# Kernel tuning notes

Measured on AMD Instinct MI355X. Metric: run time of the kernel, lower is better.

The kernel has to match this reference:

```python
import jax, jax.numpy as jnp
import numpy as np

B, S, E, H = 2, 2048, 1024, 16
D = E // H

def setup_inputs() -> dict:
    key = jax.random.key(0)
    ks = jax.random.split(key, 11)
    sc = 0.02
    inp = {
        'queries': jax.random.normal(ks[0], (B, S, E), jnp.float32),
        'keys':    jax.random.normal(ks[1], (B, S, E), jnp.float32),
        'values':  jax.random.normal(ks[2], (B, S, E), jnp.float32),
        'Wq': jax.random.normal(ks[3], (E, E), jnp.float32) * sc,
        'bq': jnp.zeros((E,), jnp.float32),
        'Wk': jax.random.normal(ks[4], (E, E), jnp.float32) * sc,
        'bk': jnp.zeros((E,), jnp.float32),
        'Wv': jax.random.normal(ks[5], (E, E), jnp.float32) * sc,
        'bv': jnp.zeros((E,), jnp.float32),
        'Wo': jax.random.normal(ks[6], (E, E), jnp.float32) * sc,
        'bo': jnp.zeros((E,), jnp.float32),
        'indicator': 0,
    }
    return inp

def reference(queries, keys, values, Wq, bq, Wk, bk, Wv, bv, Wo, bo, indicator):
    # torch Linear: y = x @ W.T + b
    q = queries @ Wq.T + bq
    k = keys    @ Wk.T + bk
    v = values  @ Wv.T + bv
    # [B,S,E] -> [B,H,S,D]
    q = q.reshape(B, S, H, D).transpose(0, 2, 1, 3)
    k = k.reshape(B, S, H, D).transpose(0, 2, 1, 3)
    v = v.reshape(B, S, H, D).transpose(0, 2, 1, 3)
    scores = jnp.einsum('bhqd,bhkd->bhqk', q, k) / jnp.sqrt(jnp.float32(D))
    w = jax.nn.sigmoid(scores)
    if indicator != 0:
        w = 1.0 - w
    attn = jax.nn.softmax(w, axis=-1)  # dropout_prob=0 -> identity
    out = jnp.einsum('bhqk,bhkd->bhqd', attn, v)
    out = out.transpose(0, 2, 1, 3).reshape(B, S, E)
    return out @ Wo.T + bo
```

## Files before the change

### kernel.cpp

```cpp
#include <hip/hip_runtime.h>
#include <stdint.h>

#define Bb 2
#define Ss 2048
#define Ee 1024
#define Hh 16
#define Dd 64

typedef __bf16 bf16;
typedef __attribute__((ext_vector_type(8))) __bf16 bf16x8;
typedef __attribute__((ext_vector_type(4))) __bf16 bf16x4;
typedef __attribute__((ext_vector_type(4))) float f32x4;

#define MB (1u << 20)
#define OFF_XQ 0u
#define OFF_XK (8u * MB)
#define OFF_XV (16u * MB)
#define OFF_WQ (24u * MB)
#define OFF_WK (26u * MB)
#define OFF_WV (28u * MB)
#define OFF_WO (30u * MB)
#define OFF_Q  (32u * MB)
#define OFF_K  (40u * MB)
#define OFF_VT (48u * MB)
#define OFF_AO (56u * MB)

__device__ __forceinline__ void gll16(const void* g, void* lds) {
  __builtin_amdgcn_global_load_lds(
      (const __attribute__((address_space(1))) void*)g,
      (__attribute__((address_space(3))) void*)lds, 16, 0, 0);
}

__device__ __forceinline__ unsigned pkbf(float lo, float hi) {
  unsigned r;
  asm("v_cvt_pk_bf16_f32 %0, %1, %2" : "=v"(r) : "v"(lo), "v"(hi));
  return r;
}
#define PL32SWAP(a, b) asm("v_permlane32_swap_b32 %0, %1" : "+v"(a), "+v"(b))
#define PL16SWAP(a, b) asm("v_permlane16_swap_b32 %0, %1" : "+v"(a), "+v"(b))

__global__ __launch_bounds__(256) void convert_kernel(
    const float* __restrict__ q, const float* __restrict__ k, const float* __restrict__ v,
    const float* __restrict__ wq, const float* __restrict__ wk, const float* __restrict__ wv,
    const float* __restrict__ wo, const int* __restrict__ ind, char* __restrict__ ws)
{
  const unsigned i = blockIdx.x * 256u + threadIdx.x;
  const float* src;
  bf16* dst;
  float scale = 1.0f;
  if (i < 3145728u) {
    const unsigned a = i >> 20, j = i & 1048575u;
    src = (a == 0 ? q : a == 1 ? k : v) + (size_t)j * 4;
    dst = (bf16*)(ws + (size_t)a * (8u * MB)) + (size_t)j * 4;
  } else {
    const unsigned i2 = i - 3145728u;
    const unsigned a = i2 >> 18, j = i2 & 262143u;
    src = (a == 0 ? wq : a == 1 ? wk : a == 2 ? wv : wo) + (size_t)j * 4;
    dst = (bf16*)(ws + OFF_WQ + (size_t)a * (2u * MB)) + (size_t)j * 4;
    if (a == 0) {
      const float c1v = (*ind != 0) ? 1.442695041f : -1.442695041f;
      scale = 0.125f * c1v;
    }
  }
  const float4 f = *(const float4*)src;
  bf16x4 o;
  o[0] = (bf16)(f.x * scale);
  o[1] = (bf16)(f.y * scale);
  o[2] = (bf16)(f.z * scale);
  o[3] = (bf16)(f.w * scale);
  *(bf16x4*)dst = o;
}

template <bool TR>
__device__ __forceinline__ void gemm128_body(
    const bf16* __restrict__ A, const bf16* __restrict__ W,
    char* smem, int m0, int n0, int t, f32x4 (&acc)[4][4])
{
  char* As = smem;
  char* Bs = smem + 16384;
  const int lane = t & 63;
  const int wid = t >> 6;
  const int wm = (wid >> 1) << 6;
  const int wn = (wid & 1) << 6;
  for (int kt = 0; kt < 1024; kt += 64) {
    __syncthreads();
#pragma unroll
    for (int i = 0; i < 4; ++i) {
      const int L = i * 4096 + t * 16;
      const int r = L >> 7;
      const int c = ((L >> 4) & 7) ^ (r & 7);
      gll16(A + (size_t)(m0 + r) * 1024 + kt + c * 8, As + i * 4096 + wid * 1024);
      gll16(W + (size_t)(n0 + r) * 1024 + kt + c * 8, Bs + i * 4096 + wid * 1024);
    }
    __syncthreads();
#pragma unroll
    for (int ks = 0; ks < 2; ++ks) {
      bf16x8 af[4], bff[4];
#pragma unroll
      for (int mi = 0; mi < 4; ++mi) {
        const int r = wm + mi * 16 + (lane & 15);
        const int c = (ks * 4 + (lane >> 4)) ^ (r & 7);
        af[mi] = *(const bf16x8*)(As + r * 128 + c * 16);
      }
#pragma unroll
      for (int ni = 0; ni < 4; ++ni) {
        const int r = wn + ni * 16 + (lane & 15);
        const int c = (ks * 4 + (lane >> 4)) ^ (r & 7);
        bff[ni] = *(const bf16x8*)(Bs + r * 128 + c * 16);
      }
      __builtin_amdgcn_s_setprio(1);
#pragma unroll
      for (int mi = 0; mi < 4; ++mi)
#pragma unroll
        for (int ni = 0; ni < 4; ++ni) {
          if (TR)
            acc[mi][ni] = __builtin_amdgcn_mfma_f32_16x16x32_bf16(bff[ni], af[mi], acc[mi][ni], 0, 0, 0);
          else
            acc[mi][ni] = __builtin_amdgcn_mfma_f32_16x16x32_bf16(af[mi], bff[ni], acc[mi][ni], 0, 0, 0);
        }
      __builtin_amdgcn_s_setprio(0);
    }
  }
}

__global__ __launch_bounds__(256) void proj_gemm(
    char* __restrict__ ws, const float* __restrict__ bq,
    const float* __restrict__ bk, const float* __restrict__ bv,
    const int* __restrict__ ind)
{
  __shared__ __align__(16) char smem[32768];
  const int zi = blockIdx.z;
  const bf16* A = (const bf16*)(ws + (zi == 0 ? OFF_XQ : zi == 1 ? OFF_XK : OFF_XV));
  const bf16* W = (const bf16*)(ws + (zi == 0 ? OFF_WQ : zi == 1 ? OFF_WK : OFF_WV));
  const float* bias = zi == 0 ? bq : zi == 1 ? bk : bv;
  bf16* outp = (bf16*)(ws + (zi == 0 ? OFF_Q : zi == 1 ? OFF_K : OFF_VT));
  const float c1v = (*ind != 0) ? 1.442695041f : -1.442695041f;
  const float bscale = (zi == 0) ? 0.125f * c1v : 1.0f;
  const int t = threadIdx.x;
  const int m0 = blockIdx.y * 128, n0 = blockIdx.x * 128;
  const int lane = t & 63, wid = t >> 6;
  const int wm = (wid >> 1) << 6, wn = (wid & 1) << 6;
  const int l15 = lane & 15, g = lane >> 4;
  f32x4 acc[4][4] = {};
  if (zi == 2) {
    gemm128_body<false>(A, W, smem, m0, n0, t, acc);
#pragma unroll
    for (int ni = 0; ni < 4; ++ni) {
      const int col = n0 + wn + ni * 16 + l15;
      const float bvv = bias[col];
      const int h = col >> 6, d = col & 63;
#pragma unroll
      for (int mi = 0; mi < 4; ++mi) {
        const int row0 = m0 + wm + mi * 16 + g * 4;
        const int b = row0 >> 11, s = row0 & 2047;
        bf16x4 o;
#pragma unroll
        for (int r2 = 0; r2 < 4; ++r2) o[r2] = (bf16)(acc[mi][ni][r2] + bvv);
        *(bf16x4*)&outp[((size_t)((b * Hh + h) * Dd + d) * Ss) + s] = o;
      }
    }
  } else {
    gemm128_body<true>(A, W, smem, m0, n0, t, acc);
#pragma unroll
    for (int mi = 0; mi < 4; ++mi) {
      const int row = m0 + wm + mi * 16 + l15;
      const int b = row >> 11, s = row & 2047;
#pragma unroll
      for (int ni = 0; ni < 4; ++ni) {
        const int col0 = n0 + wn + ni * 16 + g * 4;
        const int h = col0 >> 6, d0 = col0 & 63;
        const float4 b4 = *(const float4*)&bias[col0];
        bf16x4 o;
        o[0] = (bf16)(acc[mi][ni][0] + b4.x * bscale);
        o[1] = (bf16)(acc[mi][ni][1] + b4.y * bscale);
        o[2] = (bf16)(acc[mi][ni][2] + b4.z * bscale);
        o[3] = (bf16)(acc[mi][ni][3] + b4.w * bscale);
        *(bf16x4*)&outp[((size_t)((b * Hh + h) * Ss + s) * Dd) + d0] = o;
      }
    }
  }
}

__global__ __launch_bounds__(256, 4) void attn_kernel(char* __restrict__ ws)
{
  __shared__ __align__(16) char smem[32768];
  char* Ks  = smem;
  char* Vts = smem + 16384;
  char* Os  = smem;
  const int t = threadIdx.x, lane = t & 63, wid = t >> 6;
  const int g = lane >> 4, l15 = lane & 15;
  const int lin = blockIdx.x;
  const int bh = ((lin & 7) << 2) + ((lin >> 3) & 3);
  const int q0 = (lin >> 5) << 6;
  const bf16* Qg  = (const bf16*)(ws + OFF_Q)  + (size_t)bh * Ss * Dd;
  const bf16* Kg  = (const bf16*)(ws + OFF_K)  + (size_t)bh * Ss * Dd;
  const bf16* Vtg = (const bf16*)(ws + OFF_VT) + (size_t)bh * Ss * Dd;
  bf16* AO = (bf16*)(ws + OFF_AO);

  bf16x8 qf[2];
#pragma unroll
  for (int ks = 0; ks < 2; ++ks)
    qf[ks] = *(const bf16x8*)(Qg + (size_t)(q0 + wid * 16 + l15) * Dd + ks * 32 + g * 8);

  f32x4 acc_o[4] = {};
  f32x4 acc_sum = {};
  union { unsigned u[4]; bf16x8 v; } ones_;
#pragma unroll
  for (int j = 0; j < 4; ++j) ones_.u[j] = 0x3F803F80u;

  for (int kt = 0; kt < Ss; kt += 128) {
    __syncthreads();
#pragma unroll
    for (int i = 0; i < 4; ++i) {
      const int L = i * 4096 + t * 16;
      const int r = L >> 7;
      const int c = ((L >> 4) & 7) ^ (r & 7);
      gll16(Kg + (size_t)(kt + r) * Dd + c * 8, Ks + i * 4096 + wid * 1024);
    }
#pragma unroll
    for (int i = 0; i < 4; ++i) {
      const int L = i * 4096 + t * 16;
      const int r = L >> 8;
      const int c = ((L >> 4) & 15) ^ (r & 15);
      gll16(Vtg + (size_t)r * Ss + kt + c * 8, Vts + i * 4096 + wid * 1024);
    }
    __syncthreads();

    f32x4 st[8];
#pragma unroll
    for (int ni = 0; ni < 8; ++ni)
      st[ni] = (f32x4){-0.52876637f, -0.52876637f, -0.52876637f, -0.52876637f};
    __builtin_amdgcn_s_setprio(1);
#pragma unroll
    for (int ks = 0; ks < 2; ++ks) {
#pragma unroll
      for (int ni = 0; ni < 8; ++ni) {
        const int r = ni * 16 + l15;
        const int c = (ks * 4 + g) ^ (r & 7);
        const bf16x8 kf = *(const bf16x8*)(Ks + r * 128 + c * 16);
        st[ni] = __builtin_amdgcn_mfma_f32_16x16x32_bf16(kf, qf[ks], st[ni], 0, 0, 0);
      }
    }
    __builtin_amdgcn_s_setprio(0);

#pragma unroll
    for (int kb = 0; kb < 4; ++kb) {
      float p[2][4];
#pragma unroll
      for (int e = 0; e < 2; ++e)
#pragma unroll
        for (int r2 = 0; r2 < 4; ++r2) {
          const float ex = __builtin_amdgcn_exp2f(st[2 * kb + e][r2]);
          const float tt = __builtin_amdgcn_rcpf(0.69314718f + ex);
          p[e][r2] = __builtin_amdgcn_exp2f(tt);
        }
      unsigned E0 = pkbf(p[0][0], p[0][1]);
      unsigned E1 = pkbf(p[0][2], p[0][3]);
      unsigned O0 = pkbf(p[1][0], p[1][1]);
      unsigned O1 = pkbf(p[1][2], p[1][3]);
      PL32SWAP(E0, O0);
      PL16SWAP(E0, O0);
      PL32SWAP(E1, O1);
      PL16SWAP(E1, O1);
      union { unsigned u[4]; bf16x8 v; } pb;
      pb.u[0] = E0; pb.u[1] = E1; pb.u[2] = O0; pb.u[3] = O1;
      __builtin_amdgcn_s_setprio(1);
#pragma unroll
      for (int dblk = 0; dblk < 4; ++dblk) {
        const int r = dblk * 16 + l15;
        const int c = (kb * 4 + g) ^ (r & 15);
        const bf16x8 vf = *(const bf16x8*)(Vts + r * 256 + c * 16);
        acc_o[dblk] = __builtin_amdgcn_mfma_f32_16x16x32_bf16(vf, pb.v, acc_o[dblk], 0, 0, 0);
      }
      acc_sum = __builtin_amdgcn_mfma_f32_16x16x32_bf16(ones_.v, pb.v, acc_sum, 0, 0, 0);
      __builtin_amdgcn_s_setprio(0);
    }
  }

  const float rinv = __builtin_amdgcn_rcpf(acc_sum[0]);

  __syncthreads();
  {
    const int row = wid * 16 + l15;
#pragma unroll
    for (int dblk = 0; dblk < 4; ++dblk) {
      const unsigned w0 = pkbf(acc_o[dblk][0] * rinv, acc_o[dblk][1] * rinv);
      const unsigned w1 = pkbf(acc_o[dblk][2] * rinv, acc_o[dblk][3] * rinv);
      const int cc = dblk * 2 + (g >> 1);
      char* a = Os + row * 128 + (cc ^ (row & 7)) * 16 + (g & 1) * 8;
      *(uint2*)a = make_uint2(w0, w1);
    }
  }
  __syncthreads();
  const int b = bh >> 4, h = bh & 15;
#pragma unroll
  for (int i = 0; i < 2; ++i) {
    const int L = i * 4096 + t * 16;
    const int r = L >> 7;
    const int cc = (L >> 4) & 7;
    const uint4 w = *(const uint4*)(Os + r * 128 + (cc ^ (r & 7)) * 16);
    *(uint4*)&AO[((size_t)(b * Ss + q0 + r) << 10) + h * 64 + cc * 8] = w;
  }
}

__global__ __launch_bounds__(256) void out_gemm(char* __restrict__ ws,
                                                const float* __restrict__ bo,
                                                float* __restrict__ outp)
{
  __shared__ __align__(16) char smem[24576];
  char* As = smem;
  char* Bs = smem + 16384;
  const bf16* A = (const bf16*)(ws + OFF_AO);
  const bf16* W = (const bf16*)(ws + OFF_WO);
  const int t = threadIdx.x, lane = t & 63, wid = t >> 6;
  const int l15 = lane & 15, g = lane >> 4;
  const int m0 = blockIdx.y * 128, n0 = blockIdx.x * 64;
  const int wm = (wid >> 1) << 6;
  const int wn = (wid & 1) << 5;
  f32x4 acc[4][2] = {};
  for (int kt = 0; kt < 1024; kt += 64) {
    __syncthreads();
#pragma unroll
    for (int i = 0; i < 4; ++i) {
      const int L = i * 4096 + t * 16;
      const int r = L >> 7;
      const int c = ((L >> 4) & 7) ^ (r & 7);
      gll16(A + (size_t)(m0 + r) * 1024 + kt + c * 8, As + i * 4096 + wid * 1024);
    }
#pragma unroll
    for (int i = 0; i < 2; ++i) {
      const int L = i * 4096 + t * 16;
      const int r = L >> 7;
      const int c = ((L >> 4) & 7) ^ (r & 7);
      gll16(W + (size_t)(n0 + r) * 1024 + kt + c * 8, Bs + i * 4096 + wid * 1024);
    }
    __syncthreads();
#pragma unroll
    for (int ks = 0; ks < 2; ++ks) {
      bf16x8 af[4], bff[2];
#pragma unroll
      for (int mi = 0; mi < 4; ++mi) {
        const int r = wm + mi * 16 + l15;
        const int c = (ks * 4 + g) ^ (r & 7);
        af[mi] = *(const bf16x8*)(As + r * 128 + c * 16);
      }
#pragma unroll
      for (int ni = 0; ni < 2; ++ni) {
        const int r = wn + ni * 16 + l15;
        const int c = (ks * 4 + g) ^ (r & 7);
        bff[ni] = *(const bf16x8*)(Bs + r * 128 + c * 16);
      }
      __builtin_amdgcn_s_setprio(1);
#pragma unroll
      for (int mi = 0; mi < 4; ++mi)
#pragma unroll
        for (int ni = 0; ni < 2; ++ni)
          acc[mi][ni] = __builtin_amdgcn_mfma_f32_16x16x32_bf16(bff[ni], af[mi], acc[mi][ni], 0, 0, 0);
      __builtin_amdgcn_s_setprio(0);
    }
  }
#pragma unroll
  for (int mi = 0; mi < 4; ++mi) {
    const int row = m0 + wm + mi * 16 + l15;
#pragma unroll
    for (int ni = 0; ni < 2; ++ni) {
      const int col0 = n0 + wn + ni * 16 + g * 4;
      const float4 b4 = *(const float4*)&bo[col0];
      float4 o;
      o.x = acc[mi][ni][0] + b4.x;
      o.y = acc[mi][ni][1] + b4.y;
      o.z = acc[mi][ni][2] + b4.z;
      o.w = acc[mi][ni][3] + b4.w;
      *(float4*)&outp[(size_t)row * Ee + col0] = o;
    }
  }
}

extern "C" void kernel_launch(void* const* d_in, const int* in_sizes, int n_in,
                              void* d_out, int out_size, void* d_ws, size_t ws_size,
                              hipStream_t stream) {
  (void)in_sizes; (void)n_in; (void)out_size; (void)ws_size;
  const float* queries = (const float*)d_in[0];
  const float* keys    = (const float*)d_in[1];
  const float* values  = (const float*)d_in[2];
  const float* Wq = (const float*)d_in[3];
  const float* bq = (const float*)d_in[4];
  const float* Wk = (const float*)d_in[5];
  const float* bk = (const float*)d_in[6];
  const float* Wv = (const float*)d_in[7];
  const float* bv = (const float*)d_in[8];
  const float* Wo = (const float*)d_in[9];
  const float* bo = (const float*)d_in[10];
  const int* indicator = (const int*)d_in[11];
  char* ws = (char*)d_ws;
  float* outp = (float*)d_out;

  convert_kernel<<<16384, 256, 0, stream>>>(queries, keys, values, Wq, Wk, Wv, Wo, indicator, ws);
  proj_gemm<<<dim3(8, 32, 3), 256, 0, stream>>>(ws, bq, bk, bv, indicator);
  attn_kernel<<<1024, 256, 0, stream>>>(ws);
  out_gemm<<<dim3(16, 32), 256, 0, stream>>>(ws, bo, outp);
}
```

Baseline: 240.9 us.

## Double-buffer attention K/V tiles, double queries per block, remap GEMM blocks for locality

The attention kernel now handles 128 queries per block (two 16-row query groups per wave), which halves K/V reloads per query. It double-buffers the K/V tiles in 64KB of LDS so the next tile's global-to-LDS load overlaps the current tile's compute, with one barrier per tile. Separately, the convert kernel processes four elements per thread with a quarter of the blocks, and the projection and output GEMMs remap block IDs so that consecutive workgroups spread across XCDs for better L2 locality. The cost is higher register and LDS use per block, launch bounds drop to 2 blocks per CU, and the attention grid shrinks to 512 blocks, which lowers occupancy and parallelism.

Measured after the change: 233.0 us. -3.3%, faster.

```diff
diff --git a/kernel.cpp b/kernel.cpp
--- a/kernel.cpp
+++ b/kernel.cpp
@@ -44,31 +44,35 @@
     const float* __restrict__ wq, const float* __restrict__ wk, const float* __restrict__ wv,
     const float* __restrict__ wo, const int* __restrict__ ind, char* __restrict__ ws)
 {
-  const unsigned i = blockIdx.x * 256u + threadIdx.x;
-  const float* src;
-  bf16* dst;
-  float scale = 1.0f;
-  if (i < 3145728u) {
-    const unsigned a = i >> 20, j = i & 1048575u;
-    src = (a == 0 ? q : a == 1 ? k : v) + (size_t)j * 4;
-    dst = (bf16*)(ws + (size_t)a * (8u * MB)) + (size_t)j * 4;
-  } else {
-    const unsigned i2 = i - 3145728u;
-    const unsigned a = i2 >> 18, j = i2 & 262143u;
-    src = (a == 0 ? wq : a == 1 ? wk : a == 2 ? wv : wo) + (size_t)j * 4;
-    dst = (bf16*)(ws + OFF_WQ + (size_t)a * (2u * MB)) + (size_t)j * 4;
-    if (a == 0) {
-      const float c1v = (*ind != 0) ? 1.442695041f : -1.442695041f;
-      scale = 0.125f * c1v;
-    }
-  }
-  const float4 f = *(const float4*)src;
-  bf16x4 o;
-  o[0] = (bf16)(f.x * scale);
-  o[1] = (bf16)(f.y * scale);
-  o[2] = (bf16)(f.z * scale);
-  o[3] = (bf16)(f.w * scale);
-  *(bf16x4*)dst = o;
+  const unsigned base = blockIdx.x * 256u + threadIdx.x;
+#pragma unroll
+  for (unsigned it = 0; it < 4; ++it) {
+    const unsigned i = base + it * 1048576u;
+    const float* src;
+    bf16* dst;
+    float scale = 1.0f;
+    if (i < 3145728u) {
+      const unsigned a = i >> 20, j = i & 1048575u;
+      src = (a == 0 ? q : a == 1 ? k : v) + (size_t)j * 4;
+      dst = (bf16*)(ws + (size_t)a * (8u * MB)) + (size_t)j * 4;
+    } else {
+      const unsigned i2 = i - 3145728u;
+      const unsigned a = i2 >> 18, j = i2 & 262143u;
+      src = (a == 0 ? wq : a == 1 ? wk : a == 2 ? wv : wo) + (size_t)j * 4;
+      dst = (bf16*)(ws + OFF_WQ + (size_t)a * (2u * MB)) + (size_t)j * 4;
+      if (a == 0) {
+        const float c1v = (*ind != 0) ? 1.442695041f : -1.442695041f;
+        scale = 0.125f * c1v;
+      }
+    }
+    const float4 f = *(const float4*)src;
+    bf16x4 o;
+    o[0] = (bf16)(f.x * scale);
+    o[1] = (bf16)(f.y * scale);
+    o[2] = (bf16)(f.z * scale);
+    o[3] = (bf16)(f.w * scale);
+    *(bf16x4*)dst = o;
+  }
 }
 
 template <bool TR>
@@ -137,7 +141,9 @@
   const float c1v = (*ind != 0) ? 1.442695041f : -1.442695041f;
   const float bscale = (zi == 0) ? 0.125f * c1v : 1.0f;
   const int t = threadIdx.x;
-  const int m0 = blockIdx.y * 128, n0 = blockIdx.x * 128;
+  const int wgid = blockIdx.x + blockIdx.y * 8;
+  const int nw = (wgid & 7) * 32 + (wgid >> 3);
+  const int m0 = (nw >> 3) * 128, n0 = (nw & 7) * 128;
   const int lane = t & 63, wid = t >> 6;
   const int wm = (wid >> 1) << 6, wn = (wid & 1) << 6;
   const int l15 = lane & 15, g = lane >> 4;
@@ -181,55 +187,66 @@
   }
 }
 
-__global__ __launch_bounds__(256, 4) void attn_kernel(char* __restrict__ ws)
+__global__ __launch_bounds__(256, 2) void attn_kernel(char* __restrict__ ws)
 {
-  __shared__ __align__(16) char smem[32768];
-  char* Ks  = smem;
-  char* Vts = smem + 16384;
-  char* Os  = smem;
+  __shared__ __align__(16) char smem[65536];
+  char* Os = smem;
   const int t = threadIdx.x, lane = t & 63, wid = t >> 6;
   const int g = lane >> 4, l15 = lane & 15;
   const int lin = blockIdx.x;
-  const int bh = ((lin & 7) << 2) + ((lin >> 3) & 3);
-  const int q0 = (lin >> 5) << 6;
+  const int j = lin >> 3;
+  const int bh = ((lin & 7) << 2) + (j & 3);
+  const int q0 = (j >> 2) << 7;
   const bf16* Qg  = (const bf16*)(ws + OFF_Q)  + (size_t)bh * Ss * Dd;
   const bf16* Kg  = (const bf16*)(ws + OFF_K)  + (size_t)bh * Ss * Dd;
   const bf16* Vtg = (const bf16*)(ws + OFF_VT) + (size_t)bh * Ss * Dd;
   bf16* AO = (bf16*)(ws + OFF_AO);
 
-  bf16x8 qf[2];
-#pragma unroll
-  for (int ks = 0; ks < 2; ++ks)
-    qf[ks] = *(const bf16x8*)(Qg + (size_t)(q0 + wid * 16 + l15) * Dd + ks * 32 + g * 8);
-
-  f32x4 acc_o[4] = {};
-  f32x4 acc_sum = {};
+  bf16x8 qf[2][2];
+#pragma unroll
+  for (int qh = 0; qh < 2; ++qh)
+#pragma unroll
+    for (int ks = 0; ks < 2; ++ks)
+      qf[qh][ks] = *(const bf16x8*)(Qg + (size_t)(q0 + wid * 32 + qh * 16 + l15) * Dd + ks * 32 + g * 8);
+
+  f32x4 acc_o[2][4] = {};
+  f32x4 acc_sum[2] = {};
   union { unsigned u[4]; bf16x8 v; } ones_;
 #pragma unroll
-  for (int j = 0; j < 4; ++j) ones_.u[j] = 0x3F803F80u;
-
-  for (int kt = 0; kt < Ss; kt += 128) {
-    __syncthreads();
-#pragma unroll
-    for (int i = 0; i < 4; ++i) {
-      const int L = i * 4096 + t * 16;
-      const int r = L >> 7;
-      const int c = ((L >> 4) & 7) ^ (r & 7);
-      gll16(Kg + (size_t)(kt + r) * Dd + c * 8, Ks + i * 4096 + wid * 1024);
-    }
-#pragma unroll
-    for (int i = 0; i < 4; ++i) {
-      const int L = i * 4096 + t * 16;
-      const int r = L >> 8;
-      const int c = ((L >> 4) & 15) ^ (r & 15);
-      gll16(Vtg + (size_t)r * Ss + kt + c * 8, Vts + i * 4096 + wid * 1024);
-    }
-    __syncthreads();
-
-    f32x4 st[8];
-#pragma unroll
-    for (int ni = 0; ni < 8; ++ni)
-      st[ni] = (f32x4){-0.52876637f, -0.52876637f, -0.52876637f, -0.52876637f};
+  for (int jj = 0; jj < 4; ++jj) ones_.u[jj] = 0x3F803F80u;
+
+#define STAGE_KV(kt_, buf_)                                                         \
+  {                                                                                  \
+    char* Kb = (buf_);                                                               \
+    char* Vb = (buf_) + 16384;                                                       \
+    _Pragma("unroll")                                                                \
+    for (int i = 0; i < 4; ++i) {                                                    \
+      const int L = i * 4096 + t * 16;                                               \
+      const int rk = L >> 7;                                                         \
+      const int ck = ((L >> 4) & 7) ^ (rk & 7);                                      \
+      gll16(Kg + (size_t)((kt_) + rk) * Dd + ck * 8, Kb + i * 4096 + wid * 1024);    \
+      const int rv = L >> 8;                                                         \
+      const int cv = ((L >> 4) & 15) ^ (rv & 15);                                    \
+      gll16(Vtg + (size_t)rv * Ss + (kt_) + cv * 8, Vb + i * 4096 + wid * 1024);     \
+    }                                                                                \
+  }
+
+  STAGE_KV(0, smem);
+  __syncthreads();
+
+  for (int ti = 0; ti < 16; ++ti) {
+    char* cur = smem + (ti & 1) * 32768;
+    char* nxt = smem + ((ti & 1) ^ 1) * 32768;
+    if (ti < 15) STAGE_KV((ti + 1) * 128, nxt);
+    char* Ks = cur;
+    char* Vts = cur + 16384;
+
+    f32x4 st[2][8];
+#pragma unroll
+    for (int qh = 0; qh < 2; ++qh)
+#pragma unroll
+      for (int ni = 0; ni < 8; ++ni)
+        st[qh][ni] = (f32x4){-0.52876637f, -0.52876637f, -0.52876637f, -0.52876637f};
     __builtin_amdgcn_s_setprio(1);
 #pragma unroll
     for (int ks = 0; ks < 2; ++ks) {
@@ -238,54 +255,63 @@
         const int r = ni * 16 + l15;
         const int c = (ks * 4 + g) ^ (r & 7);
         const bf16x8 kf = *(const bf16x8*)(Ks + r * 128 + c * 16);
-        st[ni] = __builtin_amdgcn_mfma_f32_16x16x32_bf16(kf, qf[ks], st[ni], 0, 0, 0);
+        st[0][ni] = __builtin_amdgcn_mfma_f32_16x16x32_bf16(kf, qf[0][ks], st[0][ni], 0, 0, 0);
+        st[1][ni] = __builtin_amdgcn_mfma_f32_16x16x32_bf16(kf, qf[1][ks], st[1][ni], 0, 0, 0);
       }
     }
     __builtin_amdgcn_s_setprio(0);
 
 #pragma unroll
     for (int kb = 0; kb < 4; ++kb) {
-      float p[2][4];
-#pragma unroll
-      for (int e = 0; e < 2; ++e)
-#pragma unroll
-        for (int r2 = 0; r2 < 4; ++r2) {
-          const float ex = __builtin_amdgcn_exp2f(st[2 * kb + e][r2]);
-          const float tt = __builtin_amdgcn_rcpf(0.69314718f + ex);
-          p[e][r2] = __builtin_amdgcn_exp2f(tt);
-        }
-      unsigned E0 = pkbf(p[0][0], p[0][1]);
-      unsigned E1 = pkbf(p[0][2], p[0][3]);
-      unsigned O0 = pkbf(p[1][0], p[1][1]);
-      unsigned O1 = pkbf(p[1][2], p[1][3]);
-      PL32SWAP(E0, O0);
-      PL16SWAP(E0, O0);
-      PL32SWAP(E1, O1);
-      PL16SWAP(E1, O1);
-      union { unsigned u[4]; bf16x8 v; } pb;
-      pb.u[0] = E0; pb.u[1] = E1; pb.u[2] = O0; pb.u[3] = O1;
+      union { unsigned u[4]; bf16x8 v; } pb[2];
+#pragma unroll
+      for (int qh = 0; qh < 2; ++qh) {
+        float p[2][4];
+#pragma unroll
+        for (int e = 0; e < 2; ++e)
+#pragma unroll
+          for (int r2 = 0; r2 < 4; ++r2) {
+            const float ex = __builtin_amdgcn_exp2f(st[qh][2 * kb + e][r2]);
+            const float tt = __builtin_amdgcn_rcpf(0.69314718f + ex);
+            p[e][r2] = __builtin_amdgcn_exp2f(tt);
+          }
+        unsigned E0 = pkbf(p[0][0], p[0][1]);
+        unsigned E1 = pkbf(p[0][2], p[0][3]);
+        unsigned O0 = pkbf(p[1][0], p[1][1]);
+        unsigned O1 = pkbf(p[1][2], p[1][3]);
+        PL32SWAP(E0, O0);
+        PL16SWAP(E0, O0);
+        PL32SWAP(E1, O1);
+        PL16SWAP(E1, O1);
+        pb[qh].u[0] = E0; pb[qh].u[1] = E1; pb[qh].u[2] = O0; pb[qh].u[3] = O1;
+      }
       __builtin_amdgcn_s_setprio(1);
 #pragma unroll
       for (int dblk = 0; dblk < 4; ++dblk) {
         const int r = dblk * 16 + l15;
         const int c = (kb * 4 + g) ^ (r & 15);
         const bf16x8 vf = *(const bf16x8*)(Vts + r * 256 + c * 16);
-        acc_o[dblk] = __builtin_amdgcn_mfma_f32_16x16x32_bf16(vf, pb.v, acc_o[dblk], 0, 0, 0);
-      }
-      acc_sum = __builtin_amdgcn_mfma_f32_16x16x32_bf16(ones_.v, pb.v, acc_sum, 0, 0, 0);
+        acc_o[0][dblk] = __builtin_amdgcn_mfma_f32_16x16x32_bf16(vf, pb[0].v, acc_o[0][dblk], 0, 0, 0);
+        acc_o[1][dblk] = __builtin_amdgcn_mfma_f32_16x16x32_bf16(vf, pb[1].v, acc_o[1][dblk], 0, 0, 0);
+      }
+      acc_sum[0] = __builtin_amdgcn_mfma_f32_16x16x32_bf16(ones_.v, pb[0].v, acc_sum[0], 0, 0, 0);
+      acc_sum[1] = __builtin_amdgcn_mfma_f32_16x16x32_bf16(ones_.v, pb[1].v, acc_sum[1], 0, 0, 0);
       __builtin_amdgcn_s_setprio(0);
     }
-  }
-
-  const float rinv = __builtin_amdgcn_rcpf(acc_sum[0]);
-
-  __syncthreads();
-  {
-    const int row = wid * 16 + l15;
+    __syncthreads();
+  }
+#undef STAGE_KV
+
+  const float rinv[2] = {__builtin_amdgcn_rcpf(acc_sum[0][0]),
+                         __builtin_amdgcn_rcpf(acc_sum[1][0])};
+
+#pragma unroll
+  for (int qh = 0; qh < 2; ++qh) {
+    const int row = wid * 32 + qh * 16 + l15;
 #pragma unroll
     for (int dblk = 0; dblk < 4; ++dblk) {
-      const unsigned w0 = pkbf(acc_o[dblk][0] * rinv, acc_o[dblk][1] * rinv);
-      const unsigned w1 = pkbf(acc_o[dblk][2] * rinv, acc_o[dblk][3] * rinv);
+      const unsigned w0 = pkbf(acc_o[qh][dblk][0] * rinv[qh], acc_o[qh][dblk][1] * rinv[qh]);
+      const unsigned w1 = pkbf(acc_o[qh][dblk][2] * rinv[qh], acc_o[qh][dblk][3] * rinv[qh]);
       const int cc = dblk * 2 + (g >> 1);
       char* a = Os + row * 128 + (cc ^ (row & 7)) * 16 + (g & 1) * 8;
       *(uint2*)a = make_uint2(w0, w1);
@@ -294,7 +320,7 @@
   __syncthreads();
   const int b = bh >> 4, h = bh & 15;
 #pragma unroll
-  for (int i = 0; i < 2; ++i) {
+  for (int i = 0; i < 4; ++i) {
     const int L = i * 4096 + t * 16;
     const int r = L >> 7;
     const int cc = (L >> 4) & 7;
@@ -314,7 +340,9 @@
   const bf16* W = (const bf16*)(ws + OFF_WO);
   const int t = threadIdx.x, lane = t & 63, wid = t >> 6;
   const int l15 = lane & 15, g = lane >> 4;
-  const int m0 = blockIdx.y * 128, n0 = blockIdx.x * 64;
+  const int wgid = blockIdx.x + blockIdx.y * 16;
+  const int nw = (wgid & 7) * 64 + (wgid >> 3);
+  const int m0 = (nw >> 4) * 128, n0 = (nw & 15) * 64;
   const int wm = (wid >> 1) << 6;
   const int wn = (wid & 1) << 5;
   f32x4 acc[4][2] = {};
@@ -395,8 +423,8 @@
   char* ws = (char*)d_ws;
   float* outp = (float*)d_out;
 
-  convert_kernel<<<16384, 256, 0, stream>>>(queries, keys, values, Wq, Wk, Wv, Wo, indicator, ws);
+  convert_kernel<<<4096, 256, 0, stream>>>(queries, keys, values, Wq, Wk, Wv, Wo, indicator, ws);
   proj_gemm<<<dim3(8, 32, 3), 256, 0, stream>>>(ws, bq, bk, bv, indicator);
-  attn_kernel<<<1024, 256, 0, stream>>>(ws);
+  attn_kernel<<<512, 256, 0, stream>>>(ws);
   out_gemm<<<dim3(16, 32), 256, 0, stream>>>(ws, bo, outp);
 }
```
